# Kernel tuning notes

Measured on AMD Instinct MI355X. Metric: run time of the kernel, lower is better.

The kernel has to match this reference:

```python
import jax, jax.numpy as jnp
import numpy as np

EPS = 1e-6

def setup_inputs() -> dict:
    key = jax.random.key(0)
    k1, k2, k3 = jax.random.split(key, 3)
    B, D, V = 8, 4096, 32000
    hidden_states = jax.random.normal(k1, (B, D), dtype=jnp.float32)
    norm_weight = jax.random.normal(k2, (D,), dtype=jnp.float32)
    lm_head_weight = jax.random.normal(k3, (V, D), dtype=jnp.float32) * (D ** -0.5)
    return {"hidden_states": hidden_states, "norm_weight": norm_weight,
            "lm_head_weight": lm_head_weight}

def reference(hidden_states, norm_weight, lm_head_weight):
    # RMSNorm: x * rsqrt(mean(x^2) + eps) * gamma
    var = jnp.mean(jnp.square(hidden_states), axis=-1, keepdims=True)
    h = hidden_states * jax.lax.rsqrt(var + EPS) * norm_weight  # [B, D]
    # vocab projection (GEMV per row): logits [B, V]
    logits = jnp.einsum('bd,vd->bv', h, lm_head_weight)
    # top-1 token, matching torch.topk(logits.float(), 1) -> indices [B, 1]
    token = jnp.argmax(logits.astype(jnp.float32), axis=-1, keepdims=True)
    return token
```

## Files before the change

kernel.cpp:

```cpp
#include <hip/hip_runtime.h>
#include <stdint.h>


#define D 4096
#define BATCH 8
#define VOCAB 32000
#define VT 8
#define NGROUPS (VOCAB / VT)
#define NBLK 512
#define EPS 1e-6f

typedef unsigned long long u64;

__global__ __launch_bounds__(256) void rmsnorm_k(const float* __restrict__ x,
                                                 const float* __restrict__ g,
                                                 float* __restrict__ h) {
    const int b = blockIdx.x;
    const int t = threadIdx.x;
    const int wave = t >> 6, lane = t & 63;
    const float* xr = x + b * D;

    float4 xv[4];
    float s = 0.f;
#pragma unroll
    for (int i = 0; i < 4; ++i) {
        xv[i] = *(const float4*)(xr + i * 1024 + t * 4);
        s += xv[i].x * xv[i].x + xv[i].y * xv[i].y + xv[i].z * xv[i].z + xv[i].w * xv[i].w;
    }
#pragma unroll
    for (int m = 1; m < 64; m <<= 1) s += __shfl_xor(s, m, 64);

    __shared__ float wsum[4];
    if (lane == 0) wsum[wave] = s;
    __syncthreads();
    const float tot = wsum[0] + wsum[1] + wsum[2] + wsum[3];
    const float rs = rsqrtf(tot * (1.f / (float)D) + EPS);

#pragma unroll
    for (int i = 0; i < 4; ++i) {
        const int d = i * 1024 + t * 4;
        const float4 gv = *(const float4*)(g + d);
        float4 o;
        o.x = xv[i].x * rs * gv.x;
        o.y = xv[i].y * rs * gv.y;
        o.z = xv[i].z * rs * gv.z;
        o.w = xv[i].w * rs * gv.w;
        *(float4*)(h + b * D + d) = o;
    }
}

__global__ __launch_bounds__(256) void gemv_argmax_k(const float* __restrict__ W,
                                                     const float* __restrict__ h,
                                                     u64* __restrict__ partial) {
    const int lane = threadIdx.x & 63;
    const int wave = threadIdx.x >> 6;
    const int wid = blockIdx.x * 4 + wave;
    const int nw = gridDim.x * 4;

    u64 best = 0ull;

    for (int grp = wid; grp < NGROUPS; grp += nw) {
        const int v0 = grp * VT;
        const float* Wb = W + (size_t)v0 * D;

        float acc[64];
#pragma unroll
        for (int i = 0; i < 64; ++i) acc[i] = 0.f;

#pragma unroll 1
        for (int c = 0; c < 16; ++c) {
            const int d = c * 256 + lane * 4;
            float4 hv[8];
#pragma unroll
            for (int b = 0; b < 8; ++b) hv[b] = *(const float4*)(h + b * D + d);
#pragma unroll
            for (int vi = 0; vi < 8; ++vi) {
                const float4 wv = *(const float4*)(Wb + vi * D + d);
#pragma unroll
                for (int b = 0; b < 8; ++b) {
                    acc[b * 8 + vi] += wv.x * hv[b].x + wv.y * hv[b].y +
                                       wv.z * hv[b].z + wv.w * hv[b].w;
                }
            }
        }

#pragma unroll
        for (int s = 0; s < 6; ++s) {
            const int m = 1 << s;
            const bool bit = (lane & m) != 0;
#pragma unroll
            for (int u = 0; u < (64 >> (s + 1)); ++u) {
                const float a = acc[2 * u];
                const float c2 = acc[2 * u + 1];
                const float keep = bit ? c2 : a;
                const float send = bit ? a : c2;
                acc[u] = keep + __shfl_xor(send, m, 64);
            }
        }

        const float logit = acc[0];
        const int vidx = v0 + (lane & 7);
        const uint32_t fb = __float_as_uint(logit);
        const uint32_t key = (fb & 0x80000000u) ? ~fb : (fb | 0x80000000u);
        const u64 pk = ((u64)key << 32) | (uint32_t)(~(uint32_t)vidx);
        best = (pk > best) ? pk : best;
    }

#pragma unroll
    for (int m = 1; m <= 4; m <<= 1) {
        const u64 o = __shfl_xor(best, m, 64);
        if (o > best) best = o;
    }

    __shared__ u64 lb[4][8];
    if ((lane & 7) == 0) lb[wave][lane >> 3] = best;
    __syncthreads();
    if (threadIdx.x < 8) {
        const u64 m0 = lb[0][threadIdx.x], m1 = lb[1][threadIdx.x];
        const u64 m2 = lb[2][threadIdx.x], m3 = lb[3][threadIdx.x];
        const u64 a = m0 > m1 ? m0 : m1;
        const u64 b2 = m2 > m3 ? m2 : m3;
        partial[(size_t)blockIdx.x * 8 + threadIdx.x] = a > b2 ? a : b2;
    }
}

__global__ __launch_bounds__(512) void finalize_k(const u64* __restrict__ partial,
                                                  int* __restrict__ out, int nblk) {
    const int b = threadIdx.x >> 6;
    const int lane = threadIdx.x & 63;
    u64 best = 0ull;
    for (int p = lane; p < nblk; p += 64) {
        const u64 x = partial[(size_t)p * 8 + b];
        if (x > best) best = x;
    }
#pragma unroll
    for (int m = 1; m < 64; m <<= 1) {
        const u64 o = __shfl_xor(best, m, 64);
        if (o > best) best = o;
    }
    if (lane == 0) out[b] = (int)(~(uint32_t)best);
}

extern "C" void kernel_launch(void* const* d_in, const int* in_sizes, int n_in,
                              void* d_out, int out_size, void* d_ws, size_t ws_size,
                              hipStream_t stream) {
    const float* x = (const float*)d_in[0];
    const float* g = (const float*)d_in[1];
    const float* W = (const float*)d_in[2];
    int* out = (int*)d_out;

    float* h = (float*)d_ws;
    u64* partial = (u64*)((char*)d_ws + BATCH * D * sizeof(float));

    rmsnorm_k<<<BATCH, 256, 0, stream>>>(x, g, h);
    gemv_argmax_k<<<NBLK, 256, 0, stream>>>(W, h, partial);
    finalize_k<<<1, 512, 0, stream>>>(partial, out, NBLK);
}
```

Baseline: 154.4 us.

## Use one vocab group per wave with double-buffered nontemporal weight loads

Shrinks vocab tile per wave from 8 to 4 rows and launches 2000 blocks so each wave handles exactly one group, replacing the grid-stride loop. Weight loads are software double-buffered across chunks and issued as nontemporal loads, so memory fetches overlap the FMA work and the streamed weights do not pollute the caches. The reduction tree and argmax packing are adapted to the 32-accumulator layout. Each wave now reloads h more often relative to the weight rows it processes, and the larger grid increases the partial-result count that finalize must scan.

New measurement: 135.8 us. 12.1% less time.

```diff
diff --git a/kernel.cpp b/kernel.cpp
--- a/kernel.cpp
+++ b/kernel.cpp
@@ -5,12 +5,13 @@
 #define D 4096
 #define BATCH 8
 #define VOCAB 32000
-#define VT 8
+#define VT 4
 #define NGROUPS (VOCAB / VT)
-#define NBLK 512
+#define NBLK 2000
 #define EPS 1e-6f
 
 typedef unsigned long long u64;
+typedef float f32x4 __attribute__((ext_vector_type(4)));
 
 __global__ __launch_bounds__(256) void rmsnorm_k(const float* __restrict__ x,
                                                  const float* __restrict__ g,
@@ -20,11 +21,11 @@
     const int wave = t >> 6, lane = t & 63;
     const float* xr = x + b * D;
 
-    float4 xv[4];
+    f32x4 xv[4];
     float s = 0.f;
 #pragma unroll
     for (int i = 0; i < 4; ++i) {
-        xv[i] = *(const float4*)(xr + i * 1024 + t * 4);
+        xv[i] = *(const f32x4*)(xr + i * 1024 + t * 4);
         s += xv[i].x * xv[i].x + xv[i].y * xv[i].y + xv[i].z * xv[i].z + xv[i].w * xv[i].w;
     }
 #pragma unroll
@@ -39,13 +40,13 @@
 #pragma unroll
     for (int i = 0; i < 4; ++i) {
         const int d = i * 1024 + t * 4;
-        const float4 gv = *(const float4*)(g + d);
-        float4 o;
+        const f32x4 gv = *(const f32x4*)(g + d);
+        f32x4 o;
         o.x = xv[i].x * rs * gv.x;
         o.y = xv[i].y * rs * gv.y;
         o.z = xv[i].z * rs * gv.z;
         o.w = xv[i].w * rs * gv.w;
-        *(float4*)(h + b * D + d) = o;
+        *(f32x4*)(h + b * D + d) = o;
     }
 }
 
@@ -54,66 +55,81 @@
                                                      u64* __restrict__ partial) {
     const int lane = threadIdx.x & 63;
     const int wave = threadIdx.x >> 6;
-    const int wid = blockIdx.x * 4 + wave;
-    const int nw = gridDim.x * 4;
+    const int grp = blockIdx.x * 4 + wave;
+    const int v0 = grp * VT;
+    const float* Wb = W + (size_t)v0 * D;
 
-    u64 best = 0ull;
+    float acc[32];
+#pragma unroll
+    for (int i = 0; i < 32; ++i) acc[i] = 0.f;
 
-    for (int grp = wid; grp < NGROUPS; grp += nw) {
-        const int v0 = grp * VT;
-        const float* Wb = W + (size_t)v0 * D;
+    f32x4 bufA[VT], bufB[VT];
+    const int dl = lane * 4;
 
-        float acc[64];
-#pragma unroll
-        for (int i = 0; i < 64; ++i) acc[i] = 0.f;
+#define LOADW(BUF, c)                                                           \
+    {                                                                           \
+        const int _d = (c) * 256 + dl;                                          \
+        _Pragma("unroll")                                                       \
+        for (int vi = 0; vi < VT; ++vi)                                         \
+            BUF[vi] = __builtin_nontemporal_load((const f32x4*)(Wb + vi * D + _d)); \
+    }
 
+#define COMPUTE(BUF, c)                                                         \
+    {                                                                           \
+        const int _d = (c) * 256 + dl;                                          \
+        _Pragma("unroll")                                                       \
+        for (int b = 0; b < 8; ++b) {                                           \
+            const f32x4 hv = *(const f32x4*)(h + b * D + _d);                   \
+            _Pragma("unroll")                                                   \
+            for (int vi = 0; vi < VT; ++vi)                                     \
+                acc[b * VT + vi] += BUF[vi].x * hv.x + BUF[vi].y * hv.y +       \
+                                    BUF[vi].z * hv.z + BUF[vi].w * hv.w;        \
+        }                                                                       \
+    }
+
+    LOADW(bufA, 0)
 #pragma unroll 1
-        for (int c = 0; c < 16; ++c) {
-            const int d = c * 256 + lane * 4;
-            float4 hv[8];
-#pragma unroll
-            for (int b = 0; b < 8; ++b) hv[b] = *(const float4*)(h + b * D + d);
-#pragma unroll
-            for (int vi = 0; vi < 8; ++vi) {
-                const float4 wv = *(const float4*)(Wb + vi * D + d);
-#pragma unroll
-                for (int b = 0; b < 8; ++b) {
-                    acc[b * 8 + vi] += wv.x * hv[b].x + wv.y * hv[b].y +
-                                       wv.z * hv[b].z + wv.w * hv[b].w;
-                }
-            }
-        }
+    for (int c = 0; c < 16; c += 2) {
+        LOADW(bufB, c + 1)
+        COMPUTE(bufA, c)
+        LOADW(bufA, (c + 2 < 16 ? c + 2 : 15))
+        COMPUTE(bufB, c + 1)
+    }
+#undef LOADW
+#undef COMPUTE
 
 #pragma unroll
-        for (int s = 0; s < 6; ++s) {
-            const int m = 1 << s;
-            const bool bit = (lane & m) != 0;
+    for (int s = 0; s < 5; ++s) {
+        const int m = 1 << s;
+        const bool bit = (lane & m) != 0;
 #pragma unroll
-            for (int u = 0; u < (64 >> (s + 1)); ++u) {
-                const float a = acc[2 * u];
-                const float c2 = acc[2 * u + 1];
-                const float keep = bit ? c2 : a;
-                const float send = bit ? a : c2;
-                acc[u] = keep + __shfl_xor(send, m, 64);
-            }
+        for (int u = 0; u < (32 >> (s + 1)); ++u) {
+            const float a = acc[2 * u];
+            const float c2 = acc[2 * u + 1];
+            const float keep = bit ? c2 : a;
+            const float send = bit ? a : c2;
+            acc[u] = keep + __shfl_xor(send, m, 64);
         }
+    }
+    float logit = acc[0] + __shfl_xor(acc[0], 32, 64);
 
-        const float logit = acc[0];
-        const int vidx = v0 + (lane & 7);
-        const uint32_t fb = __float_as_uint(logit);
-        const uint32_t key = (fb & 0x80000000u) ? ~fb : (fb | 0x80000000u);
-        const u64 pk = ((u64)key << 32) | (uint32_t)(~(uint32_t)vidx);
-        best = (pk > best) ? pk : best;
-    }
+    const int vidx = v0 + (lane & 3);
+    const uint32_t fb = __float_as_uint(logit);
+    const uint32_t key = (fb & 0x80000000u) ? ~fb : (fb | 0x80000000u);
+    u64 best = ((u64)key << 32) | (uint32_t)(~(uint32_t)vidx);
 
 #pragma unroll
-    for (int m = 1; m <= 4; m <<= 1) {
+    for (int m = 1; m <= 2; m <<= 1) {
         const u64 o = __shfl_xor(best, m, 64);
+        if (o > best) best = o;
+    }
+    {
+        const u64 o = __shfl_xor(best, 32, 64);
         if (o > best) best = o;
     }
 
     __shared__ u64 lb[4][8];
-    if ((lane & 7) == 0) lb[wave][lane >> 3] = best;
+    if (lane < 32 && (lane & 3) == 0) lb[wave][lane >> 2] = best;
     __syncthreads();
     if (threadIdx.x < 8) {
         const u64 m0 = lb[0][threadIdx.x], m1 = lb[1][threadIdx.x];
```
